# Kernel tuning notes

Hardware: AMD Instinct MI355X
Metric: run time of the kernel (lower is better)

The kernel has to match this reference:

```python
import jax, jax.numpy as jnp
import numpy as np

E_EDGES = 100000   # number of original edges (edge tokens)
M_PAIRS = 1000000  # number of edge-edge (line-graph) pairs
IN_DIM = 128
H = 8   # num_heads
D = 16  # out_dim per head


def setup_inputs() -> dict:
    key = jax.random.key(0)
    ks = jax.random.split(key, 8)
    edge_attr = jax.random.normal(ks[0], (E_EDGES, IN_DIM), dtype=jnp.float32)
    edge_edge_index = jax.random.randint(ks[1], (2, M_PAIRS), 0, E_EDGES, dtype=jnp.int64)
    s = 1.0 / np.sqrt(IN_DIM)  # xavier-ish scale
    Wq = jax.random.normal(ks[2], (IN_DIM, H * D), dtype=jnp.float32) * s
    Wk = jax.random.normal(ks[3], (IN_DIM, H * D), dtype=jnp.float32) * s
    Wv = jax.random.normal(ks[4], (IN_DIM, H * D), dtype=jnp.float32) * s
    bq = jnp.zeros((H * D,), dtype=jnp.float32)
    bk = jnp.zeros((H * D,), dtype=jnp.float32)
    bv = jnp.zeros((H * D,), dtype=jnp.float32)
    Aw = jax.random.normal(ks[5], (D, H), dtype=jnp.float32) * (1.0 / np.sqrt(D))
    return {"edge_attr": edge_attr, "edge_edge_index": edge_edge_index,
            "Wq": Wq, "bq": bq, "Wk": Wk, "bk": bk, "Wv": Wv, "bv": bv, "Aw": Aw}


def reference(edge_attr, edge_edge_index, Wq, bq, Wk, bk, Wv, bv, Aw):
    E = edge_attr.shape[0]
    # Q/K/V projections, reshaped to [E, H, D]
    Qh = (edge_attr @ Wq + bq).reshape(E, H, D)
    Kh = (edge_attr @ Wk + bk).reshape(E, H, D)
    Vh = (edge_attr @ Wv + bv).reshape(E, H, D)
    src = edge_edge_index[0]
    dst = edge_edge_index[1]
    # gather + additive score over edge-edge pairs: [M, H, D]
    score_vec = Kh[src] + Qh[dst]  # act = Identity
    # einsum 'ehd,dhc->ehc' with c=1 -> [M, H]
    raw_attn = jnp.einsum('mhd,dh->mh', score_vec, Aw)
    # segment softmax grouped by destination edge
    mx = jax.ops.segment_max(raw_attn, dst, num_segments=E)  # [E, H]
    ex = jnp.exp(raw_attn - mx[dst])
    denom = jax.ops.segment_sum(ex, dst, num_segments=E)[dst] + 1e-16
    attn = ex / denom  # [M, H]; dropout p=0 -> identity
    # weighted scatter-add aggregation
    msg = Vh[src] * attn[..., None]  # [M, H, D]
    edge_out = jax.ops.segment_sum(msg, dst, num_segments=E)  # [E, H, D]
    return edge_out
```

## Files before the change

### kernel.cpp

```cpp
#include <hip/hip_runtime.h>
#include <math.h>

static constexpr int E = 100000;
static constexpr int M = 1000000;
static constexpr int NBE = (E + 255) / 256;
static constexpr int NBM = (M + 255) / 256;
static constexpr int NBP = (E + 63) / 64;
static constexpr int NBM4 = (M + 1023) / 1024;
static constexpr int CSTR = 4;

#define O_FLAG   0
#define O_WEFF   512
#define O_BKEFF  4608
#define O_BSWZ   5120
#define O_COUNTS 38400
#define O_OFFS   1640960
#define O_BSUM   2040960
#define O_BSUM2  2043008
#define O_BINOFF 2045056
#define O_GBIN   2046080
#define O_ORDER  2054272
#define O_POS    2454272
#define O_CSR    6454272
#define O_WS     10454272
#define O_VH     13654272
#define WS_NEEDED (O_VH + (size_t)E * 128 * 2)

typedef float f32x4 __attribute__((ext_vector_type(4)));
typedef short s16x8 __attribute__((ext_vector_type(8)));

__device__ __forceinline__ unsigned short f2bf(float f) {
    unsigned u = __float_as_uint(f);
    u += 0x7fffu + ((u >> 16) & 1u);
    return (unsigned short)(u >> 16);
}
__device__ __forceinline__ float bflo(unsigned u) { return __uint_as_float(u << 16); }
__device__ __forceinline__ float bfhi(unsigned u) { return __uint_as_float(u & 0xffff0000u); }

__device__ __forceinline__ int weswz(int k) { return (k ^ ((k >> 3) & 3)) << 3; }

__global__ void k_prep(const float* __restrict__ Wk, const float* __restrict__ bk,
                       const float* __restrict__ Aw, const float* __restrict__ Wv,
                       const int* __restrict__ idx32, int* __restrict__ flag,
                       float* __restrict__ weff, float* __restrict__ bkeff,
                       unsigned short* __restrict__ Bswz, uint4* __restrict__ countsz,
                       uint4* __restrict__ gbinz) {
    int bid = blockIdx.x, t = threadIdx.x;
    if (bid < NBE) {
        countsz[bid * 256 + t] = make_uint4(0, 0, 0, 0);
        return;
    }
    if (bid == NBE) {
        if (t < 128) {
            for (int h = 0; h < 8; h++) {
                float s = 0.f;
                for (int d = 0; d < 16; d++) s += Wk[t * 128 + h * 16 + d] * Aw[d * 8 + h];
                weff[t * 8 + h] = s;
            }
            if (t < 8) {
                float s = 0.f;
                for (int d = 0; d < 16; d++) s += bk[t * 16 + d] * Aw[d * 8 + t];
                bkeff[t] = s;
            }
        }
        return;
    }
    if (bid == NBE + 1) {
        gbinz[t * 2] = make_uint4(0, 0, 0, 0);
        gbinz[t * 2 + 1] = make_uint4(0, 0, 0, 0);
        if (t == 0) {
            int z = 0;
            for (int i = 0; i < 64; i++) z += (idx32[2 * i + 1] == 0) ? 1 : 0;
            *flag = (z == 64) ? 1 : 0;
        }
        return;
    }
    int p = (bid - (NBE + 2)) * 256 + t;
    int f = p >> 6, lane = p & 63;
    int c = f >> 3, tt = f & 7;
    int quad = lane >> 4, nn = lane & 15;
#pragma unroll
    for (int j = 0; j < 8; j++) {
        int k = c * 32 + quad * 8 + j;
        Bswz[p * 8 + j] = f2bf(Wv[k * 128 + tt * 16 + nn]);
    }
}

__global__ __launch_bounds__(256) void k_cp(
    const void* __restrict__ idx, const int* __restrict__ flagp,
    int* __restrict__ counts, int* __restrict__ pos,
    const float* __restrict__ A, const short* __restrict__ Bswz,
    const float* __restrict__ bv, const float* __restrict__ weff,
    const float* __restrict__ bkeff, unsigned short* __restrict__ Vh,
    float* __restrict__ wsb) {
    int bid = blockIdx.x, t = threadIdx.x;
    int r = bid % 5;
    if (r < 2) {
        int cid = (bid / 5) * 2 + r;
        if (cid >= NBM4) return;
        int base = cid * 1024 + t;
        int m0 = base, m1 = base + 256, m2 = base + 512, m3 = base + 768;
        int d0 = 0, d1 = 0, d2 = 0, d3 = 0;
        if (*flagp) {
            const long long* p = (const long long*)idx;
            if (m0 < M) d0 = (int)p[M + m0];
            if (m1 < M) d1 = (int)p[M + m1];
            if (m2 < M) d2 = (int)p[M + m2];
            if (m3 < M) d3 = (int)p[M + m3];
        } else {
            const int* p = (const int*)idx;
            if (m0 < M) d0 = p[M + m0];
            if (m1 < M) d1 = p[M + m1];
            if (m2 < M) d2 = p[M + m2];
            if (m3 < M) d3 = p[M + m3];
        }
        if (m0 < M) pos[m0] = atomicAdd(&counts[d0 * CSTR], 1);
        if (m1 < M) pos[m1] = atomicAdd(&counts[d1 * CSTR], 1);
        if (m2 < M) pos[m2] = atomicAdd(&counts[d2 * CSTR], 1);
        if (m3 < M) pos[m3] = atomicAdd(&counts[d3 * CSTR], 1);
        return;
    }
    int pid = (bid / 5) * 3 + (r - 2);
    if (pid >= NBP) return;

    __shared__ float we[1024];
    {
        int k = t >> 1;
        int off = weswz(k) + ((t & 1) << 2);
        *(float4*)&we[off] = ((const float4*)weff)[t];
    }
    __syncthreads();

    int lane = t & 63, wid = t >> 6;
    int rowbase = pid * 64 + wid * 16;
    int quad = lane >> 4, nn = lane & 15;
    int m = rowbase + nn;
    int mc = (m < E) ? m : (E - 1);

    f32x4 acc[8];
#pragma unroll
    for (int tt = 0; tt < 8; tt++) acc[tt] = (f32x4){0.f, 0.f, 0.f, 0.f};
    float p[8];
#pragma unroll
    for (int h = 0; h < 8; h++) p[h] = 0.f;

#pragma unroll
    for (int c = 0; c < 4; c++) {
        const float4* ap = (const float4*)(A + (size_t)mc * 128 + c * 32 + quad * 8);
        float4 f0 = ap[0], f1 = ap[1];
        float a[8] = {f0.x, f0.y, f0.z, f0.w, f1.x, f1.y, f1.z, f1.w};
#pragma unroll
        for (int j = 0; j < 8; j++) {
            int k = c * 32 + quad * 8 + j;
            int kb = weswz(k);
            float4 w0 = *(const float4*)&we[kb];
            float4 w1 = *(const float4*)&we[kb + 4];
            p[0] += a[j] * w0.x; p[1] += a[j] * w0.y;
            p[2] += a[j] * w0.z; p[3] += a[j] * w0.w;
            p[4] += a[j] * w1.x; p[5] += a[j] * w1.y;
            p[6] += a[j] * w1.z; p[7] += a[j] * w1.w;
        }
        s16x8 afrag;
#pragma unroll
        for (int j = 0; j < 8; j++) afrag[j] = (short)f2bf(a[j]);
#pragma unroll
        for (int tt = 0; tt < 8; tt++) {
            s16x8 bfrag = *(const s16x8*)(Bswz + (((c * 8 + tt) * 64 + lane) << 3));
            acc[tt] = __builtin_amdgcn_mfma_f32_16x16x32_bf16(afrag, bfrag, acc[tt], 0, 0, 0);
        }
    }
#pragma unroll
    for (int off = 16; off <= 32; off <<= 1)
#pragma unroll
        for (int h = 0; h < 8; h++) p[h] += __shfl_xor(p[h], off, 64);
    if (quad == 0 && m < E) {
        float4* op = (float4*)(wsb + (size_t)m * 8);
        op[0] = make_float4(__expf(p[0] + bkeff[0]), __expf(p[1] + bkeff[1]),
                            __expf(p[2] + bkeff[2]), __expf(p[3] + bkeff[3]));
        op[1] = make_float4(__expf(p[4] + bkeff[4]), __expf(p[5] + bkeff[5]),
                            __expf(p[6] + bkeff[6]), __expf(p[7] + bkeff[7]));
    }
#pragma unroll
    for (int tt = 0; tt < 8; tt++) {
        float bvc = bv[tt * 16 + nn];
#pragma unroll
        for (int rr = 0; rr < 4; rr++) {
            int row = rowbase + quad * 4 + rr;
            if (row < E)
                Vh[(size_t)row * 128 + tt * 16 + nn] = f2bf(acc[tt][rr] + bvc);
        }
    }
}

__global__ void k_scanA(int* __restrict__ counts, int* __restrict__ offs,
                        int* __restrict__ bsum, int* __restrict__ gbin) {
    __shared__ int sm[256];
    __shared__ int lh[256];
    __shared__ int bb[256];
    int tid = threadIdx.x;
    int i = blockIdx.x * 256 + tid;
    int v = (i < E) ? counts[i * CSTR] : 0;
    int n = v > 255 ? 255 : v;
    lh[tid] = 0;
    sm[tid] = v;
    __syncthreads();
    int lr = 0;
    if (i < E) lr = atomicAdd(&lh[n], 1);
    for (int off = 1; off < 256; off <<= 1) {
        int add = (tid >= off) ? sm[tid - off] : 0;
        __syncthreads();
        sm[tid] += add;
        __syncthreads();
    }
    if (i < E) offs[i] = sm[tid] - v;
    if (tid == 255) bsum[blockIdx.x] = sm[255];
    int cnt = lh[tid];
    if (cnt > 0) bb[tid] = atomicAdd(&gbin[tid * 8], cnt);
    __syncthreads();
    if (i < E) counts[i * CSTR] = ((bb[n] + lr) << 8) | n;
}

__global__ void k_scanB2(const int* __restrict__ bsum, const int* __restrict__ gbin,
                         int* __restrict__ bsum2, int* __restrict__ binoff, int nb) {
    __shared__ int sm[512];
    __shared__ int s2[256];
    int tid = threadIdx.x;
    int v = (tid < nb) ? bsum[tid] : 0;
    sm[tid] = v;
    __syncthreads();
    for (int off = 1; off < 512; off <<= 1) {
        int add = (tid >= off) ? sm[tid - off] : 0;
        __syncthreads();
        sm[tid] += add;
        __syncthreads();
    }
    bsum2[tid] = sm[tid] - v;
    int bv = 0;
    if (tid < 256) { bv = gbin[(255 - tid) * 8]; s2[tid] = bv; }
    __syncthreads();
    for (int off = 1; off < 256; off <<= 1) {
        int add = (tid < 256 && tid >= off) ? s2[tid - off] : 0;
        __syncthreads();
        if (tid < 256) s2[tid] += add;
        __syncthreads();
    }
    if (tid < 256) binoff[255 - tid] = s2[tid] - bv;
}

__global__ void k_fill(const void* __restrict__ idx, const int* __restrict__ flagp,
                       const int* __restrict__ offs, const int* __restrict__ bsum2,
                       const int* __restrict__ pos, int* __restrict__ csr,
                       const int* __restrict__ counts, const int* __restrict__ binoff,
                       int* __restrict__ order) {
    int bid = blockIdx.x, t = threadIdx.x;
    if (bid < NBM) {
        int m = bid * 256 + t;
        if (m >= M) return;
        int s, d;
        if (*flagp) {
            const long long* p = (const long long*)idx;
            s = (int)p[m]; d = (int)p[M + m];
        } else {
            const int* p = (const int*)idx;
            s = p[m]; d = p[M + m];
        }
        csr[offs[d] + bsum2[d >> 8] + pos[m]] = s;
        return;
    }
    int i = (bid - NBM) * 256 + t;
    if (i >= E) return;
    int v = counts[i * CSTR];
    order[binoff[v & 255] + (v >> 8)] = i;
}

#define ROWL(p, sidx, cond) \
    if (cond) { \
        k##p = wsb[(size_t)(sidx) * 8 + h]; \
        const uint4* vp_ = (const uint4*)(Vh + (size_t)(sidx) * 128 + (h << 4)); \
        a##p = vp_[0]; b##p = vp_[1]; \
    }

#define CONS(kk, aa, bb) { \
    float w_ = kk; \
    l += w_; \
    acc[0]  += bflo(aa.x) * w_; acc[1]  += bfhi(aa.x) * w_; \
    acc[2]  += bflo(aa.y) * w_; acc[3]  += bfhi(aa.y) * w_; \
    acc[4]  += bflo(aa.z) * w_; acc[5]  += bfhi(aa.z) * w_; \
    acc[6]  += bflo(aa.w) * w_; acc[7]  += bfhi(aa.w) * w_; \
    acc[8]  += bflo(bb.x) * w_; acc[9]  += bfhi(bb.x) * w_; \
    acc[10] += bflo(bb.y) * w_; acc[11] += bfhi(bb.y) * w_; \
    acc[12] += bflo(bb.z) * w_; acc[13] += bfhi(bb.z) * w_; \
    acc[14] += bflo(bb.w) * w_; acc[15] += bfhi(bb.w) * w_; \
}

__global__ __launch_bounds__(256) void k_seg(
    const float* __restrict__ wsb, const unsigned short* __restrict__ Vh,
    const int* __restrict__ offs, const int* __restrict__ bsum2,
    const int* __restrict__ csr, const int* __restrict__ order,
    float* __restrict__ out) {
    int t = threadIdx.x;
    int h = t & 7;
    int g = blockIdx.x * 32 + (t >> 3);
    int seg = order[g];
    int beg = offs[seg] + bsum2[seg >> 8];
    int end = (seg + 1 < E) ? (offs[seg + 1] + bsum2[(seg + 1) >> 8]) : M;
    int n = end - beg;

    float acc[16];
#pragma unroll
    for (int j = 0; j < 16; j++) acc[j] = 0.f;
    float l = 0.f;

    if (n > 0) {
        int s0 = 0, s1 = 0, s2 = 0, s3 = 0, t0 = 0, t1 = 0, t2 = 0, t3 = 0;
        float k0 = 0, k1 = 0, k2 = 0, k3 = 0;
        uint4 a0 = {}, b0 = {}, a1 = {}, b1 = {}, a2 = {}, b2 = {}, a3 = {}, b3 = {};
        s0 = csr[beg];
        if (n > 1) s1 = csr[beg + 1];
        if (n > 2) s2 = csr[beg + 2];
        if (n > 3) s3 = csr[beg + 3];
        ROWL(0, s0, true)
        ROWL(1, s1, n > 1)
        ROWL(2, s2, n > 2)
        ROWL(3, s3, n > 3)
        if (n > 4) t0 = csr[beg + 4];
        if (n > 5) t1 = csr[beg + 5];
        if (n > 6) t2 = csr[beg + 6];
        if (n > 7) t3 = csr[beg + 7];
        int i = 0;
        while (i + 4 <= n) {
            CONS(k0, a0, b0) ROWL(0, t0, i + 4 < n) if (i + 8 < n)  t0 = csr[beg + i + 8];
            CONS(k1, a1, b1) ROWL(1, t1, i + 5 < n) if (i + 9 < n)  t1 = csr[beg + i + 9];
            CONS(k2, a2, b2) ROWL(2, t2, i + 6 < n) if (i + 10 < n) t2 = csr[beg + i + 10];
            CONS(k3, a3, b3) ROWL(3, t3, i + 7 < n) if (i + 11 < n) t3 = csr[beg + i + 11];
            i += 4;
        }
        if (i < n) { CONS(k0, a0, b0) i++; }
        if (i < n) { CONS(k1, a1, b1) i++; }
        if (i < n) { CONS(k2, a2, b2) }
    }
    float inv = 1.0f / (l + 1e-16f);
    float4* op = (float4*)(out + (size_t)seg * 128 + h * 16);
#pragma unroll
    for (int j = 0; j < 4; j++)
        op[j] = make_float4(acc[4 * j] * inv, acc[4 * j + 1] * inv,
                            acc[4 * j + 2] * inv, acc[4 * j + 3] * inv);
}

extern "C" void kernel_launch(void* const* d_in, const int* in_sizes, int n_in,
                              void* d_out, int out_size, void* d_ws, size_t ws_size,
                              hipStream_t stream) {
    const float* edge_attr = (const float*)d_in[0];
    const void*  eei       = d_in[1];
    const float* Wk = (const float*)d_in[4];
    const float* bk = (const float*)d_in[5];
    const float* Wv = (const float*)d_in[6];
    const float* bv = (const float*)d_in[7];
    const float* Aw = (const float*)d_in[8];
    float* out = (float*)d_out;

    if (ws_size < WS_NEEDED) return;

    char* ws = (char*)d_ws;
    int*   flag   = (int*)(ws + O_FLAG);
    float* weff   = (float*)(ws + O_WEFF);
    float* bkeff  = (float*)(ws + O_BKEFF);
    unsigned short* Bswz = (unsigned short*)(ws + O_BSWZ);
    int*   counts = (int*)(ws + O_COUNTS);
    int*   offs   = (int*)(ws + O_OFFS);
    int*   bsum   = (int*)(ws + O_BSUM);
    int*   bsum2  = (int*)(ws + O_BSUM2);
    int*   binoff = (int*)(ws + O_BINOFF);
    int*   gbin   = (int*)(ws + O_GBIN);
    int*   order  = (int*)(ws + O_ORDER);
    int*   pos    = (int*)(ws + O_POS);
    int*   csr    = (int*)(ws + O_CSR);
    float* wsb    = (float*)(ws + O_WS);
    unsigned short* Vh = (unsigned short*)(ws + O_VH);

    k_prep<<<NBE + 10, 256, 0, stream>>>(Wk, bk, Aw, Wv, (const int*)eei, flag,
                                         weff, bkeff, Bswz, (uint4*)counts,
                                         (uint4*)gbin);
    k_cp<<<5 * 521, 256, 0, stream>>>(eei, flag, counts, pos, edge_attr,
                                      (const short*)Bswz, bv, weff, bkeff, Vh, wsb);
    k_scanA<<<NBE, 256, 0, stream>>>(counts, offs, bsum, gbin);
    k_scanB2<<<1, 512, 0, stream>>>(bsum, gbin, bsum2, binoff, NBE);
    k_fill<<<NBM + NBE, 256, 0, stream>>>(eei, flag, offs, bsum2, pos, csr,
                                          counts, binoff, order);
    k_seg<<<E / 32, 256, 0, stream>>>(wsb, Vh, offs, bsum2, csr, order, out);
}
```

Before: 252.0 us.

## Privatize destination-count atomics per XCC and parallelize weff precompute

```diff
diff --git a/kernel.cpp b/kernel.cpp
--- a/kernel.cpp
+++ b/kernel.cpp
@@ -7,23 +7,26 @@
 static constexpr int NBM = (M + 255) / 256;
 static constexpr int NBP = (E + 63) / 64;
 static constexpr int NBM4 = (M + 1023) / 1024;
-static constexpr int CSTR = 4;
+static constexpr int XC = 8;
+static constexpr int NBZ = (XC * E / 4 + 1023) / 1024;
+
+#define XCC_GETREG_IMM 6164
 
 #define O_FLAG   0
 #define O_WEFF   512
 #define O_BKEFF  4608
 #define O_BSWZ   5120
 #define O_COUNTS 38400
-#define O_OFFS   1640960
-#define O_BSUM   2040960
-#define O_BSUM2  2043008
-#define O_BINOFF 2045056
-#define O_GBIN   2046080
-#define O_ORDER  2054272
-#define O_POS    2454272
-#define O_CSR    6454272
-#define O_WS     10454272
-#define O_VH     13654272
+#define O_OFFS   3238400
+#define O_BSUM   3638400
+#define O_BSUM2  3640448
+#define O_BINOFF 3642496
+#define O_GBIN   3643520
+#define O_ORDER  3651712
+#define O_POS    4051712
+#define O_CSR    8051712
+#define O_WS     12051712
+#define O_VH     15251712
 #define WS_NEEDED (O_VH + (size_t)E * 128 * 2)
 
 typedef float f32x4 __attribute__((ext_vector_type(4)));
@@ -46,36 +49,46 @@
                        unsigned short* __restrict__ Bswz, uint4* __restrict__ countsz,
                        uint4* __restrict__ gbinz) {
     int bid = blockIdx.x, t = threadIdx.x;
-    if (bid < NBE) {
-        countsz[bid * 256 + t] = make_uint4(0, 0, 0, 0);
+    if (bid < NBZ) {
+        uint4 z = make_uint4(0, 0, 0, 0);
+#pragma unroll
+        for (int j = 0; j < 4; j++) {
+            int i4 = (bid * 4 + j) * 256 + t;
+            if (i4 < XC * E / 4) countsz[i4] = z;
+        }
         return;
     }
-    if (bid == NBE) {
-        if (t < 128) {
-            for (int h = 0; h < 8; h++) {
-                float s = 0.f;
-                for (int d = 0; d < 16; d++) s += Wk[t * 128 + h * 16 + d] * Aw[d * 8 + h];
-                weff[t * 8 + h] = s;
-            }
-            if (t < 8) {
-                float s = 0.f;
-                for (int d = 0; d < 16; d++) s += bk[t * 16 + d] * Aw[d * 8 + t];
-                bkeff[t] = s;
-            }
+    if (bid == NBZ) {
+        __shared__ float sAw[128];
+        if (t < 128) sAw[t] = Aw[t];
+        __syncthreads();
+#pragma unroll
+        for (int j = 0; j < 4; j++) {
+            int o = t + 256 * j;
+            int row = o >> 3, h = o & 7;
+            float s = 0.f;
+#pragma unroll
+            for (int d = 0; d < 16; d++) s += Wk[row * 128 + h * 16 + d] * sAw[d * 8 + h];
+            weff[o] = s;
+        }
+        if (t < 8) {
+            float s = 0.f;
+            for (int d = 0; d < 16; d++) s += bk[t * 16 + d] * sAw[d * 8 + t];
+            bkeff[t] = s;
         }
         return;
     }
-    if (bid == NBE + 1) {
-        gbinz[t * 2] = make_uint4(0, 0, 0, 0);
-        gbinz[t * 2 + 1] = make_uint4(0, 0, 0, 0);
+    if (bid == NBZ + 1) {
+        uint4 z = make_uint4(0, 0, 0, 0);
+        gbinz[t] = z; gbinz[t + 256] = z;
         if (t == 0) {
-            int z = 0;
-            for (int i = 0; i < 64; i++) z += (idx32[2 * i + 1] == 0) ? 1 : 0;
-            *flag = (z == 64) ? 1 : 0;
+            int zc = 0;
+            for (int i = 0; i < 64; i++) zc += (idx32[2 * i + 1] == 0) ? 1 : 0;
+            *flag = (zc == 64) ? 1 : 0;
         }
         return;
     }
-    int p = (bid - (NBE + 2)) * 256 + t;
+    int p = (bid - (NBZ + 2)) * 256 + t;
     int f = p >> 6, lane = p & 63;
     int c = f >> 3, tt = f & 7;
     int quad = lane >> 4, nn = lane & 15;
@@ -98,6 +111,9 @@
     if (r < 2) {
         int cid = (bid / 5) * 2 + r;
         if (cid >= NBM4) return;
+        unsigned xcc = __builtin_amdgcn_s_getreg(XCC_GETREG_IMM) & (XC - 1);
+        int* cb = counts + (size_t)xcc * E;
+        unsigned xtag = xcc << 28;
         int base = cid * 1024 + t;
         int m0 = base, m1 = base + 256, m2 = base + 512, m3 = base + 768;
         int d0 = 0, d1 = 0, d2 = 0, d3 = 0;
@@ -114,10 +130,14 @@
             if (m2 < M) d2 = p[M + m2];
             if (m3 < M) d3 = p[M + m3];
         }
-        if (m0 < M) pos[m0] = atomicAdd(&counts[d0 * CSTR], 1);
-        if (m1 < M) pos[m1] = atomicAdd(&counts[d1 * CSTR], 1);
-        if (m2 < M) pos[m2] = atomicAdd(&counts[d2 * CSTR], 1);
-        if (m3 < M) pos[m3] = atomicAdd(&counts[d3 * CSTR], 1);
+        if (m0 < M) pos[m0] = (int)(xtag | (unsigned)__hip_atomic_fetch_add(
+                                 &cb[d0], 1, __ATOMIC_RELAXED, __HIP_MEMORY_SCOPE_WORKGROUP));
+        if (m1 < M) pos[m1] = (int)(xtag | (unsigned)__hip_atomic_fetch_add(
+                                 &cb[d1], 1, __ATOMIC_RELAXED, __HIP_MEMORY_SCOPE_WORKGROUP));
+        if (m2 < M) pos[m2] = (int)(xtag | (unsigned)__hip_atomic_fetch_add(
+                                 &cb[d2], 1, __ATOMIC_RELAXED, __HIP_MEMORY_SCOPE_WORKGROUP));
+        if (m3 < M) pos[m3] = (int)(xtag | (unsigned)__hip_atomic_fetch_add(
+                                 &cb[d3], 1, __ATOMIC_RELAXED, __HIP_MEMORY_SCOPE_WORKGROUP));
         return;
     }
     int pid = (bid / 5) * 3 + (r - 2);
@@ -199,7 +219,19 @@
     __shared__ int bb[256];
     int tid = threadIdx.x;
     int i = blockIdx.x * 256 + tid;
-    int v = (i < E) ? counts[i * CSTR] : 0;
+    int tot = 0;
+    if (i < E) {
+        int pre[XC];
+#pragma unroll
+        for (int x = 0; x < XC; x++) {
+            int cx = counts[(size_t)x * E + i];
+            pre[x] = tot;
+            tot += cx;
+        }
+#pragma unroll
+        for (int x = 1; x < XC; x++) counts[(size_t)x * E + i] = pre[x];
+    }
+    int v = (i < E) ? tot : 0;
     int n = v > 255 ? 255 : v;
     lh[tid] = 0;
     sm[tid] = v;
@@ -217,7 +249,7 @@
     int cnt = lh[tid];
     if (cnt > 0) bb[tid] = atomicAdd(&gbin[tid * 8], cnt);
     __syncthreads();
-    if (i < E) counts[i * CSTR] = ((bb[n] + lr) << 8) | n;
+    if (i < E) counts[i] = ((bb[n] + lr) << 8) | n;
 }
 
 __global__ void k_scanB2(const int* __restrict__ bsum, const int* __restrict__ gbin,
@@ -264,12 +296,16 @@
             const int* p = (const int*)idx;
             s = p[m]; d = p[M + m];
         }
-        csr[offs[d] + bsum2[d >> 8] + pos[m]] = s;
+        int pk = pos[m];
+        unsigned xcc = ((unsigned)pk) >> 28;
+        int rank = pk & 0x0FFFFFFF;
+        int sb = xcc ? counts[(size_t)xcc * E + d] : 0;
+        csr[offs[d] + bsum2[d >> 8] + sb + rank] = s;
         return;
     }
     int i = (bid - NBM) * 256 + t;
     if (i >= E) return;
-    int v = counts[i * CSTR];
+    int v = counts[i];
     order[binoff[v & 255] + (v >> 8)] = i;
 }
 
@@ -378,7 +414,7 @@
     float* wsb    = (float*)(ws + O_WS);
     unsigned short* Vh = (unsigned short*)(ws + O_VH);
 
-    k_prep<<<NBE + 10, 256, 0, stream>>>(Wk, bk, Aw, Wv, (const int*)eei, flag,
+    k_prep<<<NBZ + 10, 256, 0, stream>>>(Wk, bk, Aw, Wv, (const int*)eei, flag,
                                          weff, bkeff, Bswz, (uint4*)counts,
                                          (uint4*)gbin);
     k_cp<<<5 * 521, 256, 0, stream>>>(eei, flag, counts, pos, edge_attr,
```

Result: no change. 255.6 us (+1.4%).
